# Optimization experiments

Measured on AMD Instinct MI355X. Metric: run time of the kernel, lower is better.

The kernel has to match this reference:

```python
import math
import jax, jax.numpy as jnp
import numpy as np

B, N, D, H, R = 2, 2048, 1024, 16, 32
DK = D // H


def _alibi_bias(n_heads, n_tokens):
    # faithful port of _alibi_slopes + alibi_bias (n_heads, n_tokens are static ints)
    def pow2slopes(n):
        start = 2.0 ** (-(2.0 ** (-(math.log2(n) - 3))))
        return [start * (start ** i) for i in range(n)]
    if math.log2(n_heads).is_integer():
        vals = pow2slopes(n_heads)
    else:
        closest = 2 ** math.floor(math.log2(n_heads))
        vals = pow2slopes(closest) + pow2slopes(2 * closest)[0::2][: n_heads - closest]
    slopes = jnp.asarray(vals, dtype=jnp.float32).reshape(1, n_heads, 1, 1)
    i = jnp.arange(n_tokens).reshape(1, 1, n_tokens, 1)
    j = jnp.arange(n_tokens).reshape(1, 1, 1, n_tokens)
    dist = jnp.maximum(j - i, 0).astype(jnp.float32)
    return -slopes * dist  # [1, h, n, n]


def setup_inputs() -> dict:
    key = jax.random.key(0)
    ks = jax.random.split(key, 6)
    x = jax.random.normal(ks[0], (B, N, D), dtype=jnp.float32)
    s = 0.02
    Wq = jax.random.normal(ks[1], (D, D), dtype=jnp.float32) * s
    Wk = jax.random.normal(ks[2], (D, D), dtype=jnp.float32) * s
    Wv = jax.random.normal(ks[3], (D, D), dtype=jnp.float32) * s
    Wproj = jax.random.normal(ks[4], (D, D), dtype=jnp.float32) * s
    # orthogonal init of U [dk, r] via QR (orthonormal columns)
    U, _ = jnp.linalg.qr(jax.random.normal(ks[5], (DK, R), dtype=jnp.float32))
    # additive causal mask (0 on/below diagonal, -1e9 above)
    i = jnp.arange(N).reshape(N, 1)
    j = jnp.arange(N).reshape(1, N)
    mask = jnp.where(j <= i, 0.0, -1e9).astype(jnp.float32).reshape(1, 1, N, N)
    return {"x": x, "Wq": Wq, "Wk": Wk, "Wv": Wv, "U": U, "Wproj": Wproj,
            "mask": mask, "h": H, "rel_bias_tokens": N}


def reference(x, Wq, Wk, Wv, U, Wproj, mask, h, rel_bias_tokens):
    b, n, d = x.shape
    dk = d // h
    scale = 1.0 / math.sqrt(dk)  # note: scaled by sqrt(dk), not sqrt(r)

    def proj_qk(y):  # [b,n,d] -> [b,h,n,r]
        return jnp.einsum('bnhk,kr->bhnr', y.reshape(b, n, h, dk), U)

    q = proj_qk(x @ Wq.T)
    k = proj_qk(x @ Wk.T)
    v = (x @ Wv.T).reshape(b, n, h, dk).transpose(0, 2, 1, 3)  # [b,h,n,dk]

    att = jnp.einsum('bhqr,bhkr->bhqk', q, k) * scale  # [b,h,n,n]
    bias = _alibi_bias(h, rel_bias_tokens)[:, :, -n:, :]
    att = att + bias + mask
    z = jnp.einsum('bhqk,bhkd->bhqd', jax.nn.softmax(att, axis=-1), v)
    z = z.transpose(0, 2, 1, 3).reshape(b, n, h * dk)
    out = z @ Wproj.T  # dropout is identity in eval
    return out
```

## Files before the change

### kernel.cpp

```cpp
#include <hip/hip_runtime.h>
#include <math.h>

#define B_   2
#define N_   2048
#define D_   1024
#define H_   16
#define R_   32
#define DK_  64
#define HR_  512
#define QC_  2048
#define M_   4096

typedef __attribute__((ext_vector_type(8))) short  bf16x8;
typedef __attribute__((ext_vector_type(4))) float  f32x4;
typedef unsigned short ushort_t;

__device__ __forceinline__ unsigned short bf16_rne(float f) {
    unsigned u = __float_as_uint(f);
    unsigned r = (u + 0x7FFFu + ((u >> 16) & 1u)) >> 16;
    return (unsigned short)r;
}
__device__ __forceinline__ float bf16_to_f(unsigned short h) {
    return __uint_as_float(((unsigned)h) << 16);
}
__device__ __forceinline__ void gload_lds16(const void* g, void* l) {
    __builtin_amdgcn_global_load_lds(
        (const __attribute__((address_space(1))) unsigned int*)g,
        (__attribute__((address_space(3))) unsigned int*)l, 16, 0, 0);
}

__global__ __launch_bounds__(256) void build_bmat2(
    const float* __restrict__ Wq, const float* __restrict__ Wk,
    const float* __restrict__ Wv, const float* __restrict__ U,
    ushort_t* __restrict__ BhT, ushort_t* __restrict__ BlT)
{
    int idx = blockIdx.x * 256 + threadIdx.x;
    int e = idx >> 10;
    int d = idx & 1023;
    float val;
    if (e < 1024) {
        const float* W = (e < 512) ? Wq : Wk;
        int eh = e & 511;
        int h = eh >> 5;
        int r = eh & 31;
        float acc = 0.f;
        #pragma unroll
        for (int kk = 0; kk < DK_; ++kk)
            acc = fmaf(W[(size_t)(h*DK_ + kk)*D_ + d], U[kk*R_ + r], acc);
        val = (e < 512) ? acc * 0.125f : acc;
    } else {
        val = Wv[(size_t)(e - 1024)*D_ + d];
    }
    unsigned short h16 = bf16_rne(val);
    BhT[idx] = h16;
    BlT[idx] = bf16_rne(val - bf16_to_f(h16));
}

__global__ __launch_bounds__(256) void cvt_hl(
    const float* __restrict__ src, ushort_t* __restrict__ dh,
    ushort_t* __restrict__ dl)
{
    int i = blockIdx.x * 256 + threadIdx.x;
    float4 v = ((const float4*)src)[i];
    unsigned short h0 = bf16_rne(v.x), h1 = bf16_rne(v.y),
                   h2 = bf16_rne(v.z), h3 = bf16_rne(v.w);
    ((ushort4*)dh)[i] = make_ushort4(h0, h1, h2, h3);
    ((ushort4*)dl)[i] = make_ushort4(bf16_rne(v.x - bf16_to_f(h0)),
                                     bf16_rne(v.y - bf16_to_f(h1)),
                                     bf16_rne(v.z - bf16_to_f(h2)),
                                     bf16_rne(v.w - bf16_to_f(h3)));
}

template<int EPI>
__global__ __launch_bounds__(256) void gemm_hl(
    const ushort_t* __restrict__ Ah, const ushort_t* __restrict__ Al,
    const ushort_t* __restrict__ Bh, const ushort_t* __restrict__ Bl,
    float* __restrict__ C,
    ushort_t* __restrict__ Qh, ushort_t* __restrict__ Ql,
    ushort_t* __restrict__ Kh, ushort_t* __restrict__ Kl,
    float* __restrict__ Vf,
    int M, int Nn, int K)
{
    __shared__ __attribute__((aligned(16))) ushort_t lds[4][128][32];
    int nb = Nn >> 7;
    int bx = blockIdx.x % nb, by = blockIdx.x / nb;
    int m0 = by << 7, n0 = bx << 7;
    int tid = threadIdx.x;
    int wave = tid >> 6, lane = tid & 63;
    int wr = wave >> 1, wc = wave & 1;

    const ushort_t* gsrc = (wave == 0) ? Ah : (wave == 1) ? Al
                         : (wave == 2) ? Bh : Bl;
    int row0 = (wave < 2) ? m0 : n0;
    int rloc  = lane >> 2;
    int kslot = lane & 3;

    f32x4 acc[4][4];
    #pragma unroll
    for (int i = 0; i < 4; ++i)
        #pragma unroll
        for (int j = 0; j < 4; ++j)
            acc[i][j] = (f32x4){0.f, 0.f, 0.f, 0.f};

    char* ldsb = (char*)&lds[0][0][0];

    for (int k0 = 0; k0 < K; k0 += 32) {
        #pragma unroll
        for (int seg = 0; seg < 8; ++seg) {
            int r = seg*16 + rloc;
            int ksw = (kslot << 4) ^ (((r >> 1) & 3) << 4);
            const ushort_t* gp = gsrc + (size_t)(row0 + r)*K + k0 + (ksw >> 1);
            gload_lds16(gp, ldsb + wave*8192 + seg*1024);
        }
        asm volatile("s_waitcnt vmcnt(0)" ::: "memory");
        __syncthreads();

        bf16x8 a_h[4], a_l[4];
        #pragma unroll
        for (int mf = 0; mf < 4; ++mf) {
            int r  = wr*64 + mf*16 + (lane & 15);
            int kb = ((lane >> 4) << 4) ^ (((r >> 1) & 3) << 4);
            a_h[mf] = *(const bf16x8*)(ldsb +        r*64 + kb);
            a_l[mf] = *(const bf16x8*)(ldsb + 8192 + r*64 + kb);
        }
        #pragma unroll
        for (int nf = 0; nf < 4; ++nf) {
            int r  = wc*64 + nf*16 + (lane & 15);
            int kb = ((lane >> 4) << 4) ^ (((r >> 1) & 3) << 4);
            bf16x8 b_h = *(const bf16x8*)(ldsb + 16384 + r*64 + kb);
            bf16x8 b_l = *(const bf16x8*)(ldsb + 24576 + r*64 + kb);
            #pragma unroll
            for (int mf = 0; mf < 4; ++mf)
                acc[mf][nf] = __builtin_amdgcn_mfma_f32_16x16x32_bf16(
                    a_h[mf], b_h, acc[mf][nf], 0, 0, 0);
            #pragma unroll
            for (int mf = 0; mf < 4; ++mf)
                acc[mf][nf] = __builtin_amdgcn_mfma_f32_16x16x32_bf16(
                    a_h[mf], b_l, acc[mf][nf], 0, 0, 0);
            #pragma unroll
            for (int mf = 0; mf < 4; ++mf)
                acc[mf][nf] = __builtin_amdgcn_mfma_f32_16x16x32_bf16(
                    a_l[mf], b_h, acc[mf][nf], 0, 0, 0);
        }
        __syncthreads();
    }
    int cr = (lane >> 4) << 2;
    int cc = lane & 15;
    #pragma unroll
    for (int mf = 0; mf < 4; ++mf)
        #pragma unroll
        for (int nf = 0; nf < 4; ++nf) {
            int rr = m0 + wr*64 + mf*16 + cr;
            int c  = n0 + wc*64 + nf*16 + cc;
            #pragma unroll
            for (int rg = 0; rg < 4; ++rg) {
                float v = acc[mf][nf][rg];
                if (EPI == 0) {
                    C[(size_t)(rr + rg)*Nn + c] = v;
                } else {
                    int t = rr + rg;
                    if (n0 < 512) {
                        unsigned short h16 = bf16_rne(v);
                        Qh[(size_t)t*HR_ + c] = h16;
                        Ql[(size_t)t*HR_ + c] = bf16_rne(v - bf16_to_f(h16));
                    } else if (n0 < 1024) {
                        unsigned short h16 = bf16_rne(v);
                        Kh[(size_t)t*HR_ + c - 512] = h16;
                        Kl[(size_t)t*HR_ + c - 512] = bf16_rne(v - bf16_to_f(h16));
                    } else {
                        Vf[(size_t)t*D_ + c - 1024] = v;
                    }
                }
            }
        }
}

__global__ __launch_bounds__(256) void cvtVT(
    const float* __restrict__ Vf, ushort_t* __restrict__ VTh,
    ushort_t* __restrict__ VTl)
{
    __shared__ float Ls[64][65];
    int blk = blockIdx.x;
    int bh = blk >> 5, kvt = blk & 31;
    int b = bh >> 4, hh = bh & 15;
    int tid = threadIdx.x;
    int t0 = b*N_ + kvt*64;
    int u = tid >> 4, v = tid & 15;
    #pragma unroll
    for (int p = 0; p < 4; ++p) {
        int r = p*16 + u;
        int c4 = v*4;
        float4 x4 = *(const float4*)(Vf + (size_t)(t0 + r)*D_ + hh*64 + c4);
        Ls[r][c4+0] = x4.x; Ls[r][c4+1] = x4.y;
        Ls[r][c4+2] = x4.z; Ls[r][c4+3] = x4.w;
    }
    __syncthreads();
    #pragma unroll
    for (int p = 0; p < 4; ++p) {
        int d = p*16 + u;
        int kvb = v*4;
        float f0 = Ls[kvb+0][d], f1 = Ls[kvb+1][d],
              f2 = Ls[kvb+2][d], f3 = Ls[kvb+3][d];
        unsigned short h0 = bf16_rne(f0), h1 = bf16_rne(f1),
                       h2 = bf16_rne(f2), h3 = bf16_rne(f3);
        size_t o = ((size_t)(bh*64 + d))*N_ + kvt*64 + kvb;
        *(ushort4*)(VTh + o) = make_ushort4(h0, h1, h2, h3);
        *(ushort4*)(VTl + o) = make_ushort4(bf16_rne(f0 - bf16_to_f(h0)),
                                            bf16_rne(f1 - bf16_to_f(h1)),
                                            bf16_rne(f2 - bf16_to_f(h2)),
                                            bf16_rne(f3 - bf16_to_f(h3)));
    }
}

__global__ __launch_bounds__(256) void attn5(
    const ushort_t* __restrict__ Qbh, const ushort_t* __restrict__ Qbl,
    const ushort_t* __restrict__ Kbh, const ushort_t* __restrict__ Kbl,
    const ushort_t* __restrict__ VTh, const ushort_t* __restrict__ VTl,
    ushort_t* __restrict__ zh, ushort_t* __restrict__ zl)
{
    const float MCONST = 12.0f;
    __shared__ float mg[2][64][36];
    __shared__ float ots[2][16][68];
    int bIdx = blockIdx.x;
    int qt = 31 - (bIdx >> 5);
    int bh = bIdx & 31;
    int b = bh >> 4, hh = bh & 15;
    int tid = threadIdx.x;
    int wave = tid >> 6, lane = tid & 63;
    int c = lane & 15, g = lane >> 4;
    int qw = wave & 1, par = wave >> 1;
    int qbase = qt*64 + qw*32;

    bf16x8 qh[2], ql[2];
    #pragma unroll
    for (int qs = 0; qs < 2; ++qs) {
        size_t qo = ((size_t)(b*N_ + qbase + qs*16 + c))*HR_ + hh*R_ + g*8;
        qh[qs] = *(const bf16x8*)(Qbh + qo);
        ql[qs] = *(const bf16x8*)(Qbl + qo);
    }
    f32x4 acc[2][4];
    #pragma unroll
    for (int qs = 0; qs < 2; ++qs)
        #pragma unroll
        for (int ds = 0; ds < 4; ++ds)
            acc[qs][ds] = (f32x4){0.f, 0.f, 0.f, 0.f};
    float lsum[2] = {0.f, 0.f};

    int nkt = 2*qt + qw + 1;
    int kpa = 8*(c >> 2) + (c & 3);

    for (int kvt = par; kvt < nkt; kvt += 2) {
        int kv0 = kvt*32;
        bf16x8 kh[2], kl[2];
        #pragma unroll
        for (int ks = 0; ks < 2; ++ks) {
            size_t ko = ((size_t)(b*N_ + kv0 + kpa + ks*4))*HR_ + hh*R_ + g*8;
            kh[ks] = *(const bf16x8*)(Kbh + ko);
            kl[ks] = *(const bf16x8*)(Kbl + ko);
        }
        f32x4 s[2][2];
        #pragma unroll
        for (int qs = 0; qs < 2; ++qs)
            #pragma unroll
            for (int ks = 0; ks < 2; ++ks) {
                f32x4 t = (f32x4){0.f, 0.f, 0.f, 0.f};
                t = __builtin_amdgcn_mfma_f32_16x16x32_bf16(kh[ks], qh[qs], t, 0, 0, 0);
                t = __builtin_amdgcn_mfma_f32_16x16x32_bf16(kl[ks], qh[qs], t, 0, 0, 0);
                t = __builtin_amdgcn_mfma_f32_16x16x32_bf16(kh[ks], ql[qs], t, 0, 0, 0);
                s[qs][ks] = t;
            }
        bool needmask = (kv0 + 31 > qbase);
        bf16x8 pH[2], pL[2];
        #pragma unroll
        for (int qs = 0; qs < 2; ++qs) {
            int q = qbase + qs*16 + c;
            float p[8];
            #pragma unroll
            for (int ks = 0; ks < 2; ++ks)
                #pragma unroll
                for (int r = 0; r < 4; ++r) {
                    float sv = s[qs][ks][r];
                    if (needmask && (kv0 + 8*g + ks*4 + r > q)) sv = -1e30f;
                    p[ks*4 + r] = __expf(sv - MCONST);
                }
            lsum[qs] += ((p[0]+p[1]) + (p[2]+p[3])) +
                        ((p[4]+p[5]) + (p[6]+p[7]));
            #pragma unroll
            for (int j = 0; j < 8; ++j) {
                unsigned pb = __float_as_uint(p[j]);
                pH[qs][j] = (short)(pb >> 16);
                float hi = __uint_as_float(pb & 0xFFFF0000u);
                pL[qs][j] = (short)(__float_as_uint(p[j] - hi) >> 16);
            }
        }
        #pragma unroll
        for (int ds = 0; ds < 4; ++ds) {
            size_t vo = ((size_t)(bh*64 + ds*16 + c))*N_ + kv0 + g*8;
            bf16x8 vh = *(const bf16x8*)(VTh + vo);
            bf16x8 vl = *(const bf16x8*)(VTl + vo);
            #pragma unroll
            for (int qs = 0; qs < 2; ++qs) {
                acc[qs][ds] = __builtin_amdgcn_mfma_f32_16x16x32_bf16(
                    vh, pH[qs], acc[qs][ds], 0, 0, 0);
                acc[qs][ds] = __builtin_amdgcn_mfma_f32_16x16x32_bf16(
                    vh, pL[qs], acc[qs][ds], 0, 0, 0);
                acc[qs][ds] = __builtin_amdgcn_mfma_f32_16x16x32_bf16(
                    vl, pH[qs], acc[qs][ds], 0, 0, 0);
            }
        }
    }

    #pragma unroll
    for (int qs = 0; qs < 2; ++qs) {
        lsum[qs] += __shfl_xor(lsum[qs], 16);
        lsum[qs] += __shfl_xor(lsum[qs], 32);
    }

    if (par == 1) {
        #pragma unroll
        for (int qs = 0; qs < 2; ++qs)
            #pragma unroll
            for (int ds = 0; ds < 4; ++ds)
                *(float4*)(&mg[qw][lane][qs*16 + ds*4]) =
                    make_float4(acc[qs][ds][0], acc[qs][ds][1],
                                acc[qs][ds][2], acc[qs][ds][3]);
        mg[qw][lane][32] = lsum[0];
        mg[qw][lane][33] = lsum[1];
    }
    __syncthreads();
    if (par == 0) {
        #pragma unroll
        for (int qs = 0; qs < 2; ++qs) {
            float inv = 1.0f / (lsum[qs] + mg[qw][lane][32 + qs]);
            #pragma unroll
            for (int ds = 0; ds < 4; ++ds)
                #pragma unroll
                for (int rg = 0; rg < 4; ++rg)
                    acc[qs][ds][rg] = (acc[qs][ds][rg] +
                        mg[qw][lane][qs*16 + ds*4 + rg]) * inv;
        }
        #pragma unroll
        for (int qs = 0; qs < 2; ++qs) {
            #pragma unroll
            for (int ds = 0; ds < 4; ++ds)
                #pragma unroll
                for (int rg = 0; rg < 4; ++rg)
                    ots[qw][c][ds*16 + g*4 + rg] = acc[qs][ds][rg];
            int qr = lane >> 2;
            size_t trow = (size_t)(b*N_ + qbase + qs*16 + qr);
            #pragma unroll
            for (int j4 = 0; j4 < 4; ++j4) {
                int d0 = j4*16 + (lane & 3)*4;
                float4 v4 = *(const float4*)(&ots[qw][qr][d0]);
                unsigned short h0 = bf16_rne(v4.x), h1 = bf16_rne(v4.y),
                               h2 = bf16_rne(v4.z), h3 = bf16_rne(v4.w);
                *(ushort4*)(zh + trow*D_ + hh*64 + d0) =
                    make_ushort4(h0, h1, h2, h3);
                *(ushort4*)(zl + trow*D_ + hh*64 + d0) =
                    make_ushort4(bf16_rne(v4.x - bf16_to_f(h0)),
                                 bf16_rne(v4.y - bf16_to_f(h1)),
                                 bf16_rne(v4.z - bf16_to_f(h2)),
                                 bf16_rne(v4.w - bf16_to_f(h3)));
            }
        }
    }
}

extern "C" void kernel_launch(void* const* d_in, const int* in_sizes, int n_in,
                              void* d_out, int out_size, void* d_ws, size_t ws_size,
                              hipStream_t stream)
{
    (void)in_sizes; (void)n_in; (void)out_size; (void)ws_size;
    const float* x  = (const float*)d_in[0];
    const float* Wq = (const float*)d_in[1];
    const float* Wk = (const float*)d_in[2];
    const float* Wv = (const float*)d_in[3];
    const float* U  = (const float*)d_in[4];
    const float* Wp = (const float*)d_in[5];
    float* out = (float*)d_out;

    const size_t MB = 1048576;
    char* w = (char*)d_ws;
    float*    Vf  = (float*)   (w);
    ushort_t* Qbh = (ushort_t*)(w + 16*MB);
    ushort_t* Qbl = (ushort_t*)(w + 20*MB);
    ushort_t* Kbh = (ushort_t*)(w + 24*MB);
    ushort_t* Kbl = (ushort_t*)(w + 28*MB);
    ushort_t* BhT = (ushort_t*)(w + 32*MB);
    ushort_t* BlT = (ushort_t*)(w + 36*MB);
    ushort_t* wph = (ushort_t*)(w + 40*MB);
    ushort_t* wpl = (ushort_t*)(w + 42*MB);
    ushort_t* xzh = (ushort_t*)(w + 44*MB);
    ushort_t* xzl = (ushort_t*)(w + 52*MB);
    ushort_t* VTh = (ushort_t*)(w + 44*MB);
    ushort_t* VTl = (ushort_t*)(w + 52*MB);
    ushort_t* zh  = (ushort_t*)(w);
    ushort_t* zl  = (ushort_t*)(w + 8*MB);

    build_bmat2<<<dim3(8192), dim3(256), 0, stream>>>(Wq, Wk, Wv, U, BhT, BlT);
    cvt_hl<<<dim3(4096), dim3(256), 0, stream>>>(x, xzh, xzl);
    cvt_hl<<<dim3(1024), dim3(256), 0, stream>>>(Wp, wph, wpl);
    gemm_hl<1><<<dim3(512), dim3(256), 0, stream>>>(
        xzh, xzl, BhT, BlT, nullptr, Qbh, Qbl, Kbh, Kbl, Vf, M_, QC_, D_);
    cvtVT<<<dim3(1024), dim3(256), 0, stream>>>(Vf, VTh, VTl);
    attn5<<<dim3(1024), dim3(256), 0, stream>>>(
        Qbh, Qbl, Kbh, Kbl, VTh, VTl, zh, zl);
    gemm_hl<0><<<dim3(256), dim3(256), 0, stream>>>(
        zh, zl, wph, wpl, out, nullptr, nullptr, nullptr, nullptr, nullptr,
        M_, D_, D_);
}
```

Baseline: 335.1 us.

## Restructure attention into paired 32-row query tiles with 4-way KV split and prefetch

Each block now handles two complementary 32-row query tiles (qt and 63-qt), so every block does roughly equal causal work. The KV loop is split across all four waves instead of two, and the next K tile is double-buffered in registers while the current one is processed. V loads are hoisted ahead of the MFMAs. The partials from three waves are merged through shared memory, which adds extra reductions, two barriers per half and more register pressure.

```diff
diff --git a/kernel.cpp b/kernel.cpp
--- a/kernel.cpp
+++ b/kernel.cpp
@@ -212,157 +212,197 @@
     }
 }
 
-__global__ __launch_bounds__(256) void attn5(
+__device__ __forceinline__ void attn_tile(
+    int kvt, int qt, int qb, int bN, int bh, int c, int g,
+    const bf16x8 (&kh)[2], const bf16x8 (&kl)[2],
+    const bf16x8 (&qh)[2], const bf16x8 (&ql)[2],
+    const ushort_t* __restrict__ VTh, const ushort_t* __restrict__ VTl,
+    f32x4 (&acc)[2][4], float (&lsum)[2])
+{
+    const float MCONST = 12.0f;
+    int kv0 = kvt*32;
+    bf16x8 vh[4], vl[4];
+    #pragma unroll
+    for (int ds = 0; ds < 4; ++ds) {
+        size_t vo = ((size_t)(bh*64 + ds*16 + c))*N_ + kv0 + g*8;
+        vh[ds] = *(const bf16x8*)(VTh + vo);
+        vl[ds] = *(const bf16x8*)(VTl + vo);
+    }
+    f32x4 s[2][2];
+    #pragma unroll
+    for (int qs = 0; qs < 2; ++qs)
+        #pragma unroll
+        for (int ks = 0; ks < 2; ++ks) {
+            f32x4 t = (f32x4){0.f, 0.f, 0.f, 0.f};
+            t = __builtin_amdgcn_mfma_f32_16x16x32_bf16(kh[ks], qh[qs], t, 0, 0, 0);
+            t = __builtin_amdgcn_mfma_f32_16x16x32_bf16(kl[ks], qh[qs], t, 0, 0, 0);
+            t = __builtin_amdgcn_mfma_f32_16x16x32_bf16(kh[ks], ql[qs], t, 0, 0, 0);
+            s[qs][ks] = t;
+        }
+    bool needmask = (kvt == qt);
+    bf16x8 pH[2], pL[2];
+    #pragma unroll
+    for (int qs = 0; qs < 2; ++qs) {
+        int q = qb + qs*16 + c;
+        float p[8];
+        #pragma unroll
+        for (int ks = 0; ks < 2; ++ks)
+            #pragma unroll
+            for (int r = 0; r < 4; ++r) {
+                float sv = s[qs][ks][r];
+                if (needmask && (kv0 + 8*g + ks*4 + r > q)) sv = -1e30f;
+                p[ks*4 + r] = __expf(sv - MCONST);
+            }
+        lsum[qs] += ((p[0]+p[1]) + (p[2]+p[3])) + ((p[4]+p[5]) + (p[6]+p[7]));
+        #pragma unroll
+        for (int j = 0; j < 8; ++j) {
+            unsigned pb = __float_as_uint(p[j]);
+            pH[qs][j] = (short)(pb >> 16);
+            float hi = __uint_as_float(pb & 0xFFFF0000u);
+            pL[qs][j] = (short)(__float_as_uint(p[j] - hi) >> 16);
+        }
+    }
+    #pragma unroll
+    for (int ds = 0; ds < 4; ++ds)
+        #pragma unroll
+        for (int qs = 0; qs < 2; ++qs) {
+            acc[qs][ds] = __builtin_amdgcn_mfma_f32_16x16x32_bf16(
+                vh[ds], pH[qs], acc[qs][ds], 0, 0, 0);
+            acc[qs][ds] = __builtin_amdgcn_mfma_f32_16x16x32_bf16(
+                vh[ds], pL[qs], acc[qs][ds], 0, 0, 0);
+            acc[qs][ds] = __builtin_amdgcn_mfma_f32_16x16x32_bf16(
+                vl[ds], pH[qs], acc[qs][ds], 0, 0, 0);
+        }
+}
+
+__global__ __launch_bounds__(256) void attn6(
     const ushort_t* __restrict__ Qbh, const ushort_t* __restrict__ Qbl,
     const ushort_t* __restrict__ Kbh, const ushort_t* __restrict__ Kbl,
     const ushort_t* __restrict__ VTh, const ushort_t* __restrict__ VTl,
     ushort_t* __restrict__ zh, ushort_t* __restrict__ zl)
 {
-    const float MCONST = 12.0f;
-    __shared__ float mg[2][64][36];
-    __shared__ float ots[2][16][68];
+    __shared__ float mg[3][64][36];
+    __shared__ float ots[16][68];
     int bIdx = blockIdx.x;
-    int qt = 31 - (bIdx >> 5);
+    int pr = bIdx >> 5;
     int bh = bIdx & 31;
     int b = bh >> 4, hh = bh & 15;
     int tid = threadIdx.x;
     int wave = tid >> 6, lane = tid & 63;
     int c = lane & 15, g = lane >> 4;
-    int qw = wave & 1, par = wave >> 1;
-    int qbase = qt*64 + qw*32;
-
-    bf16x8 qh[2], ql[2];
-    #pragma unroll
-    for (int qs = 0; qs < 2; ++qs) {
-        size_t qo = ((size_t)(b*N_ + qbase + qs*16 + c))*HR_ + hh*R_ + g*8;
-        qh[qs] = *(const bf16x8*)(Qbh + qo);
-        ql[qs] = *(const bf16x8*)(Qbl + qo);
-    }
-    f32x4 acc[2][4];
-    #pragma unroll
-    for (int qs = 0; qs < 2; ++qs)
-        #pragma unroll
-        for (int ds = 0; ds < 4; ++ds)
-            acc[qs][ds] = (f32x4){0.f, 0.f, 0.f, 0.f};
-    float lsum[2] = {0.f, 0.f};
-
-    int nkt = 2*qt + qw + 1;
     int kpa = 8*(c >> 2) + (c & 3);
-
-    for (int kvt = par; kvt < nkt; kvt += 2) {
-        int kv0 = kvt*32;
-        bf16x8 kh[2], kl[2];
-        #pragma unroll
-        for (int ks = 0; ks < 2; ++ks) {
-            size_t ko = ((size_t)(b*N_ + kv0 + kpa + ks*4))*HR_ + hh*R_ + g*8;
-            kh[ks] = *(const bf16x8*)(Kbh + ko);
-            kl[ks] = *(const bf16x8*)(Kbl + ko);
-        }
-        f32x4 s[2][2];
+    int bN = b*N_;
+
+    #pragma unroll 1
+    for (int hf = 0; hf < 2; ++hf) {
+        int qt = hf ? pr : 63 - pr;
+        int qb = qt << 5;
+        int nkt = qt + 1;
+
+        bf16x8 qh[2], ql[2];
+        #pragma unroll
+        for (int qs = 0; qs < 2; ++qs) {
+            size_t qo = ((size_t)(bN + qb + qs*16 + c))*HR_ + hh*R_ + g*8;
+            qh[qs] = *(const bf16x8*)(Qbh + qo);
+            ql[qs] = *(const bf16x8*)(Qbl + qo);
+        }
+        f32x4 acc[2][4];
         #pragma unroll
         for (int qs = 0; qs < 2; ++qs)
             #pragma unroll
-            for (int ks = 0; ks < 2; ++ks) {
-                f32x4 t = (f32x4){0.f, 0.f, 0.f, 0.f};
-                t = __builtin_amdgcn_mfma_f32_16x16x32_bf16(kh[ks], qh[qs], t, 0, 0, 0);
-                t = __builtin_amdgcn_mfma_f32_16x16x32_bf16(kl[ks], qh[qs], t, 0, 0, 0);
-                t = __builtin_amdgcn_mfma_f32_16x16x32_bf16(kh[ks], ql[qs], t, 0, 0, 0);
-                s[qs][ks] = t;
-            }
-        bool needmask = (kv0 + 31 > qbase);
-        bf16x8 pH[2], pL[2];
+            for (int ds = 0; ds < 4; ++ds)
+                acc[qs][ds] = (f32x4){0.f, 0.f, 0.f, 0.f};
+        float lsum[2] = {0.f, 0.f};
+
+        #define LOADK(KVT, KH, KL)                                            \
+            _Pragma("unroll")                                                 \
+            for (int ks = 0; ks < 2; ++ks) {                                  \
+                size_t ko = ((size_t)(bN + (KVT)*32 + kpa + ks*4))*HR_        \
+                            + hh*R_ + g*8;                                    \
+                KH[ks] = *(const bf16x8*)(Kbh + ko);                          \
+                KL[ks] = *(const bf16x8*)(Kbl + ko);                          \
+            }
+
+        bf16x8 khA[2], klA[2], khB[2], klB[2];
+        int kvt = wave;
+        if (kvt < nkt) {
+            LOADK(kvt, khA, klA);
+            while (true) {
+                int kv2 = kvt + 4;
+                if (kv2 < nkt) { LOADK(kv2, khB, klB); }
+                attn_tile(kvt, qt, qb, bN, bh, c, g, khA, klA, qh, ql,
+                          VTh, VTl, acc, lsum);
+                if (kv2 >= nkt) break;
+                int kv3 = kv2 + 4;
+                if (kv3 < nkt) { LOADK(kv3, khA, klA); }
+                attn_tile(kv2, qt, qb, bN, bh, c, g, khB, klB, qh, ql,
+                          VTh, VTl, acc, lsum);
+                if (kv3 >= nkt) break;
+                kvt = kv3;
+            }
+        }
+        #undef LOADK
+
         #pragma unroll
         for (int qs = 0; qs < 2; ++qs) {
-            int q = qbase + qs*16 + c;
-            float p[8];
-            #pragma unroll
-            for (int ks = 0; ks < 2; ++ks)
+            lsum[qs] += __shfl_xor(lsum[qs], 16);
+            lsum[qs] += __shfl_xor(lsum[qs], 32);
+        }
+
+        if (wave != 0) {
+            int w = wave - 1;
+            #pragma unroll
+            for (int qs = 0; qs < 2; ++qs)
                 #pragma unroll
-                for (int r = 0; r < 4; ++r) {
-                    float sv = s[qs][ks][r];
-                    if (needmask && (kv0 + 8*g + ks*4 + r > q)) sv = -1e30f;
-                    p[ks*4 + r] = __expf(sv - MCONST);
+                for (int ds = 0; ds < 4; ++ds)
+                    *(float4*)(&mg[w][lane][qs*16 + ds*4]) =
+                        make_float4(acc[qs][ds][0], acc[qs][ds][1],
+                                    acc[qs][ds][2], acc[qs][ds][3]);
+            mg[w][lane][32] = lsum[0];
+            mg[w][lane][33] = lsum[1];
+        }
+        __syncthreads();
+        if (wave == 0) {
+            #pragma unroll
+            for (int qs = 0; qs < 2; ++qs) {
+                float lt = lsum[qs] + mg[0][lane][32 + qs]
+                         + mg[1][lane][32 + qs] + mg[2][lane][32 + qs];
+                float inv = 1.0f / lt;
+                #pragma unroll
+                for (int ds = 0; ds < 4; ++ds)
+                    #pragma unroll
+                    for (int rg = 0; rg < 4; ++rg)
+                        acc[qs][ds][rg] = (acc[qs][ds][rg]
+                            + mg[0][lane][qs*16 + ds*4 + rg]
+                            + mg[1][lane][qs*16 + ds*4 + rg]
+                            + mg[2][lane][qs*16 + ds*4 + rg]) * inv;
+            }
+            #pragma unroll
+            for (int qs = 0; qs < 2; ++qs) {
+                #pragma unroll
+                for (int ds = 0; ds < 4; ++ds)
+                    #pragma unroll
+                    for (int rg = 0; rg < 4; ++rg)
+                        ots[c][ds*16 + g*4 + rg] = acc[qs][ds][rg];
+                int qr = lane >> 2;
+                size_t trow = (size_t)(bN + qb + qs*16 + qr);
+                #pragma unroll
+                for (int j4 = 0; j4 < 4; ++j4) {
+                    int d0 = j4*16 + (lane & 3)*4;
+                    float4 v4 = *(const float4*)(&ots[qr][d0]);
+                    unsigned short h0 = bf16_rne(v4.x), h1 = bf16_rne(v4.y),
+                                   h2 = bf16_rne(v4.z), h3 = bf16_rne(v4.w);
+                    *(ushort4*)(zh + trow*D_ + hh*64 + d0) =
+                        make_ushort4(h0, h1, h2, h3);
+                    *(ushort4*)(zl + trow*D_ + hh*64 + d0) =
+                        make_ushort4(bf16_rne(v4.x - bf16_to_f(h0)),
+                                     bf16_rne(v4.y - bf16_to_f(h1)),
+                                     bf16_rne(v4.z - bf16_to_f(h2)),
+                                     bf16_rne(v4.w - bf16_to_f(h3)));
                 }
-            lsum[qs] += ((p[0]+p[1]) + (p[2]+p[3])) +
-                        ((p[4]+p[5]) + (p[6]+p[7]));
-            #pragma unroll
-            for (int j = 0; j < 8; ++j) {
-                unsigned pb = __float_as_uint(p[j]);
-                pH[qs][j] = (short)(pb >> 16);
-                float hi = __uint_as_float(pb & 0xFFFF0000u);
-                pL[qs][j] = (short)(__float_as_uint(p[j] - hi) >> 16);
-            }
-        }
-        #pragma unroll
-        for (int ds = 0; ds < 4; ++ds) {
-            size_t vo = ((size_t)(bh*64 + ds*16 + c))*N_ + kv0 + g*8;
-            bf16x8 vh = *(const bf16x8*)(VTh + vo);
-            bf16x8 vl = *(const bf16x8*)(VTl + vo);
-            #pragma unroll
-            for (int qs = 0; qs < 2; ++qs) {
-                acc[qs][ds] = __builtin_amdgcn_mfma_f32_16x16x32_bf16(
-                    vh, pH[qs], acc[qs][ds], 0, 0, 0);
-                acc[qs][ds] = __builtin_amdgcn_mfma_f32_16x16x32_bf16(
-                    vh, pL[qs], acc[qs][ds], 0, 0, 0);
-                acc[qs][ds] = __builtin_amdgcn_mfma_f32_16x16x32_bf16(
-                    vl, pH[qs], acc[qs][ds], 0, 0, 0);
-            }
-        }
-    }
-
-    #pragma unroll
-    for (int qs = 0; qs < 2; ++qs) {
-        lsum[qs] += __shfl_xor(lsum[qs], 16);
-        lsum[qs] += __shfl_xor(lsum[qs], 32);
-    }
-
-    if (par == 1) {
-        #pragma unroll
-        for (int qs = 0; qs < 2; ++qs)
-            #pragma unroll
-            for (int ds = 0; ds < 4; ++ds)
-                *(float4*)(&mg[qw][lane][qs*16 + ds*4]) =
-                    make_float4(acc[qs][ds][0], acc[qs][ds][1],
-                                acc[qs][ds][2], acc[qs][ds][3]);
-        mg[qw][lane][32] = lsum[0];
-        mg[qw][lane][33] = lsum[1];
-    }
-    __syncthreads();
-    if (par == 0) {
-        #pragma unroll
-        for (int qs = 0; qs < 2; ++qs) {
-            float inv = 1.0f / (lsum[qs] + mg[qw][lane][32 + qs]);
-            #pragma unroll
-            for (int ds = 0; ds < 4; ++ds)
-                #pragma unroll
-                for (int rg = 0; rg < 4; ++rg)
-                    acc[qs][ds][rg] = (acc[qs][ds][rg] +
-                        mg[qw][lane][qs*16 + ds*4 + rg]) * inv;
-        }
-        #pragma unroll
-        for (int qs = 0; qs < 2; ++qs) {
-            #pragma unroll
-            for (int ds = 0; ds < 4; ++ds)
-                #pragma unroll
-                for (int rg = 0; rg < 4; ++rg)
-                    ots[qw][c][ds*16 + g*4 + rg] = acc[qs][ds][rg];
-            int qr = lane >> 2;
-            size_t trow = (size_t)(b*N_ + qbase + qs*16 + qr);
-            #pragma unroll
-            for (int j4 = 0; j4 < 4; ++j4) {
-                int d0 = j4*16 + (lane & 3)*4;
-                float4 v4 = *(const float4*)(&ots[qw][qr][d0]);
-                unsigned short h0 = bf16_rne(v4.x), h1 = bf16_rne(v4.y),
-                               h2 = bf16_rne(v4.z), h3 = bf16_rne(v4.w);
-                *(ushort4*)(zh + trow*D_ + hh*64 + d0) =
-                    make_ushort4(h0, h1, h2, h3);
-                *(ushort4*)(zl + trow*D_ + hh*64 + d0) =
-                    make_ushort4(bf16_rne(v4.x - bf16_to_f(h0)),
-                                 bf16_rne(v4.y - bf16_to_f(h1)),
-                                 bf16_rne(v4.z - bf16_to_f(h2)),
-                                 bf16_rne(v4.w - bf16_to_f(h3)));
-            }
-        }
+            }
+        }
+        __syncthreads();
     }
 }
 
@@ -403,7 +443,7 @@
     gemm_hl<1><<<dim3(512), dim3(256), 0, stream>>>(
         xzh, xzl, BhT, BlT, nullptr, Qbh, Qbl, Kbh, Kbl, Vf, M_, QC_, D_);
     cvtVT<<<dim3(1024), dim3(256), 0, stream>>>(Vf, VTh, VTl);
-    attn5<<<dim3(1024), dim3(256), 0, stream>>>(
+    attn6<<<dim3(1024), dim3(256), 0, stream>>>(
         Qbh, Qbl, Kbh, Kbl, VTh, VTl, zh, zl);
     gemm_hl<0><<<dim3(256), dim3(256), 0, stream>>>(
         zh, zl, wph, wpl, out, nullptr, nullptr, nullptr, nullptr, nullptr,
```

Result: faster. 326.3 us (-2.6%).
